# Kernel optimization log

Hardware: AMD Instinct MI355X
Metric: run time of the kernel (lower is better)

Reference implementation:

```python
import jax, jax.numpy as jnp
import numpy as np

GUIDING_LAMBDA = 0.6
N_EXPERT = 4


def setup_inputs() -> dict:
    key = jax.random.key(0)
    ks = jax.random.split(key, 8)
    B, L, H, E = 8, 128, 768, 7
    D = 2 * (H + E + 1)  # 1552 pair-embedding dim
    s = 0.02
    return {
        "utter_repr": jax.random.normal(ks[0], (B, L, H), jnp.float32),
        "speaker_ids": jax.random.randint(ks[1], (B, L), 0, 2),
        "emo_W": jax.random.normal(ks[2], (H, E), jnp.float32) * s,
        "emo_b": jnp.zeros((E,), jnp.float32),
        "gate_W": jax.random.normal(ks[3], (D, N_EXPERT), jnp.float32) * s,
        "gate_b": jnp.zeros((N_EXPERT,), jnp.float32),
        "exp_W1": jax.random.normal(ks[4], (N_EXPERT, D, 256), jnp.float32) * s,
        "exp_b1": jnp.zeros((N_EXPERT, 256), jnp.float32),
        "exp_W2": jax.random.normal(ks[5], (N_EXPERT, 256, 2), jnp.float32) * s,
        "exp_b2": jnp.zeros((N_EXPERT, 2), jnp.float32),
    }


def reference(utter_repr, speaker_ids, emo_W, emo_b, gate_W, gate_b,
              exp_W1, exp_b1, exp_W2, exp_b2):
    B, L, H = utter_repr.shape
    flat = utter_repr.reshape(B * L, H)
    # emotion classification head (dropout = identity in eval)
    emotion_pred = flat @ emo_W + emo_b                      # [B*L, 7]
    spk = speaker_ids.reshape(B * L, 1).astype(flat.dtype)
    concat = jnp.concatenate([flat, emotion_pred, spk], axis=-1)
    concat = concat.reshape(B, L, -1)                        # [B, L, 776]
    # all (t, end_t) pairs with t <= end_t  (vectorized form of the nested loops)
    end_idx, t_idx = np.tril_indices(L)                      # P = L(L+1)/2
    pair = jnp.concatenate([concat[:, t_idx], concat[:, end_idx]], axis=-1)
    pair_flat = pair.reshape(-1, pair.shape[-1])             # [B*P, 1552]
    # gating on detached pair embedding
    gating = jax.nn.softmax(
        jax.lax.stop_gradient(pair_flat) @ gate_W + gate_b, axis=-1)
    # mechanical subtask label (speaker / emotion agreement -> 4-way one-hot)
    s_eq = speaker_ids[:, t_idx] == speaker_ids[:, end_idx]  # [B, P]
    emo = jnp.argmax(emotion_pred.reshape(B, L, -1), axis=-1)
    e_eq = emo[:, t_idx] == emo[:, end_idx]
    lbl = jnp.where(s_eq & e_eq, 0,
                    jnp.where(s_eq, 1, jnp.where(e_eq, 2, 3)))
    label = jax.nn.one_hot(lbl.reshape(-1), N_EXPERT, dtype=pair_flat.dtype)
    gating = GUIDING_LAMBDA * label + (1.0 - GUIDING_LAMBDA) * gating
    # experts: Linear(1552,256) -> Linear(256,2), no activation between
    hidden = jnp.einsum('pd,edh->eph', pair_flat, exp_W1) + exp_b1[:, None, :]
    expert_out = jnp.einsum('eph,ehc->epc', hidden, exp_W2) + exp_b2[:, None, :]
    cause_pred = jnp.einsum('pe,epc->pc', gating, expert_out)  # [B*P, 2]
    return emotion_pred, cause_pred
```

## Files before the change

kernel.cpp:

```cpp
#include <hip/hip_runtime.h>
#include <math.h>

#define B_   8
#define L_   128
#define H_   768
#define E_   7
#define NE_  4
#define HALF_ 776
#define D_   1552
#define PPB_ 8256
#define NROW_ 1024
#define EMO_OUT_ 7168

#define WEFF_OFF 0
#define BEFF_OFF 12416
#define EARG_OFF 12424
#define GLO_OFF  13448
#define GHI_OFF  17544
#define AA_OFF   21640
#define BB_OFF   29832

__global__ __launch_bounds__(256)
void k_weff(const float* __restrict__ w1,
            const float* __restrict__ w2,
            const float* __restrict__ b1,
            const float* __restrict__ b2,
            float* __restrict__ ws) {
    int idx = blockIdx.x * 256 + threadIdx.x;
    if (idx < NE_ * D_) {
        int e = idx / D_, d = idx % D_;
        const float* w1row = w1 + ((size_t)e * D_ + d) * 256;
        const float* w2e   = w2 + e * 512;
        float a0 = 0.f, a1 = 0.f;
        #pragma unroll 8
        for (int h = 0; h < 256; ++h) {
            float x = w1row[h];
            a0 += x * w2e[2 * h];
            a1 += x * w2e[2 * h + 1];
        }
        ws[WEFF_OFF + d * 8 + e * 2 + 0] = a0;
        ws[WEFF_OFF + d * 8 + e * 2 + 1] = a1;
    } else if (idx < NE_ * D_ + 8) {
        int j = idx - NE_ * D_;
        int e = j >> 1, c = j & 1;
        const float* w2e = w2 + e * 512;
        float acc = b2[e * 2 + c];
        for (int h = 0; h < 256; ++h) acc += b1[e * 256 + h] * w2e[2 * h + c];
        ws[BEFF_OFF + j] = acc;
    }
}

__global__ __launch_bounds__(64)
void k_row(const float* __restrict__ utter,
           const int*   __restrict__ spk,
           const float* __restrict__ emoW,
           const float* __restrict__ emoB,
           const float* __restrict__ gateW,
           float* __restrict__ ws,
           float* __restrict__ out) {
    int row  = blockIdx.x;
    int lane = threadIdx.x;
    const float* x = utter + (size_t)row * H_;

    float aemo[E_];
    float ag[24];
    #pragma unroll
    for (int j = 0; j < E_; ++j) aemo[j] = 0.f;
    #pragma unroll
    for (int k = 0; k < 24; ++k) ag[k] = 0.f;

    for (int d = lane; d < H_; d += 64) {
        float v = x[d];
        const float* ew = emoW + d * E_;
        #pragma unroll
        for (int j = 0; j < E_; ++j) aemo[j] += v * ew[j];
        const float* gl = gateW + d * NE_;
        const float* gh = gateW + (HALF_ + d) * NE_;
        #pragma unroll
        for (int k = 0; k < NE_; ++k) { ag[k] += v * gl[k]; ag[4 + k] += v * gh[k]; }
        const float* wl = ws + WEFF_OFF + d * 8;
        const float* wh = ws + WEFF_OFF + (HALF_ + d) * 8;
        #pragma unroll
        for (int k = 0; k < 8; ++k) { ag[8 + k] += v * wl[k]; ag[16 + k] += v * wh[k]; }
    }

    #pragma unroll
    for (int j = 0; j < E_; ++j) {
        float v = aemo[j];
        for (int o = 32; o > 0; o >>= 1) v += __shfl_xor(v, o, 64);
        aemo[j] = v + emoB[j];
    }

    if (lane == 0) {
        int best = 0; float bv = aemo[0];
        #pragma unroll
        for (int j = 1; j < E_; ++j) if (aemo[j] > bv) { bv = aemo[j]; best = j; }
        ((int*)ws)[EARG_OFF + row] = best;
        #pragma unroll
        for (int j = 0; j < E_; ++j) out[row * E_ + j] = aemo[j];
    }

    if (lane < 8) {
        float v = (lane < E_) ? aemo[lane] : (float)spk[row];
        int d = H_ + lane;
        const float* gl = gateW + d * NE_;
        const float* gh = gateW + (HALF_ + d) * NE_;
        #pragma unroll
        for (int k = 0; k < NE_; ++k) { ag[k] += v * gl[k]; ag[4 + k] += v * gh[k]; }
        const float* wl = ws + WEFF_OFF + d * 8;
        const float* wh = ws + WEFF_OFF + (HALF_ + d) * 8;
        #pragma unroll
        for (int k = 0; k < 8; ++k) { ag[8 + k] += v * wl[k]; ag[16 + k] += v * wh[k]; }
    }

    #pragma unroll
    for (int k = 0; k < 24; ++k) {
        float v = ag[k];
        for (int o = 32; o > 0; o >>= 1) v += __shfl_xor(v, o, 64);
        ag[k] = v;
    }

    if (lane == 0) {
        #pragma unroll
        for (int k = 0; k < NE_; ++k) {
            ws[GLO_OFF + row * 4 + k] = ag[k];
            ws[GHI_OFF + row * 4 + k] = ag[4 + k];
        }
        #pragma unroll
        for (int k = 0; k < 8; ++k) {
            ws[AA_OFF + row * 8 + k] = ag[8 + k];
            ws[BB_OFF + row * 8 + k] = ag[16 + k];
        }
    }
}

__global__ __launch_bounds__(128)
void k_pair(const int* __restrict__ spk,
            const float* __restrict__ ws,
            const float* __restrict__ gate_b,
            float* __restrict__ out) {
    int b   = blockIdx.x >> 7;
    int end = blockIdx.x & 127;
    int t   = threadIdx.x;
    if (t > end) return;

    int rt = b * L_ + t;
    int re = b * L_ + end;

    float gb0 = gate_b[0], gb1 = gate_b[1], gb2 = gate_b[2], gb3 = gate_b[3];
    const float* beff = ws + BEFF_OFF;
    float be[8];
    #pragma unroll
    for (int k = 0; k < 8; ++k) be[k] = beff[k];

    const float* glo = ws + GLO_OFF + rt * 4;
    const float* ghi = ws + GHI_OFF + re * 4;
    float lg[NE_];
    lg[0] = glo[0] + ghi[0] + gb0;
    lg[1] = glo[1] + ghi[1] + gb1;
    lg[2] = glo[2] + ghi[2] + gb2;
    lg[3] = glo[3] + ghi[3] + gb3;

    float m = fmaxf(fmaxf(lg[0], lg[1]), fmaxf(lg[2], lg[3]));
    float ex[NE_], s = 0.f;
    #pragma unroll
    for (int k = 0; k < NE_; ++k) { ex[k] = expf(lg[k] - m); s += ex[k]; }
    float inv = 0.4f / s;

    const int* earg = (const int*)ws + EARG_OFF;
    bool seq = (spk[rt] == spk[re]);
    bool eeq = (earg[rt] == earg[re]);
    int lbl = (seq && eeq) ? 0 : (seq ? 1 : (eeq ? 2 : 3));

    const float* A  = ws + AA_OFF + rt * 8;
    const float* Bv = ws + BB_OFF + re * 8;

    float o0 = 0.f, o1 = 0.f;
    #pragma unroll
    for (int e = 0; e < NE_; ++e) {
        float g = ex[e] * inv + ((e == lbl) ? 0.6f : 0.f);
        o0 += g * (A[e * 2 + 0] + Bv[e * 2 + 0] + be[e * 2 + 0]);
        o1 += g * (A[e * 2 + 1] + Bv[e * 2 + 1] + be[e * 2 + 1]);
    }

    int p = ((end * (end + 1)) >> 1) + t;
    float* cp = out + EMO_OUT_ + ((size_t)b * PPB_ + p) * 2;
    cp[0] = o0;
    cp[1] = o1;
}

extern "C" void kernel_launch(void* const* d_in, const int* in_sizes, int n_in,
                              void* d_out, int out_size, void* d_ws, size_t ws_size,
                              hipStream_t stream) {
    const float* utter = (const float*)d_in[0];
    const int*   spk   = (const int*)  d_in[1];
    const float* emoW  = (const float*)d_in[2];
    const float* emoB  = (const float*)d_in[3];
    const float* gateW = (const float*)d_in[4];
    const float* gateB = (const float*)d_in[5];
    const float* w1    = (const float*)d_in[6];
    const float* b1    = (const float*)d_in[7];
    const float* w2    = (const float*)d_in[8];
    const float* b2    = (const float*)d_in[9];

    float* ws  = (float*)d_ws;
    float* out = (float*)d_out;

    k_weff<<<(NE_ * D_ + 8 + 255) / 256, 256, 0, stream>>>(w1, w2, b1, b2, ws);
    k_row<<<NROW_, 64, 0, stream>>>(utter, spk, emoW, emoB, gateW, ws, out);
    k_pair<<<B_ * L_, 128, 0, stream>>>(spk, ws, gateB, out);
}
```

Measured before the change: 102.4 us.

## Split weff reduction across threads and vectorize row and pair loads

k_weff now gives each (expert, d) output four threads that each cover a quarter of the hidden dimension with float4 loads, then combine the partial sums through shared memory. The bias-folding block is split across eight lanes with a shuffle reduction. k_row processes four contiguous features per lane using float4 loads of the inputs and weights, and k_pair reads its workspace data as float4. The aim is to cut the serial per-thread loop in k_weff, which reads the 6 MB W1 with a strided, uncoalesced pattern, and to reduce the number of load instructions. The cost is higher register use in k_row.

```diff
diff --git a/kernel.cpp b/kernel.cpp
--- a/kernel.cpp
+++ b/kernel.cpp
@@ -20,33 +20,58 @@
 #define AA_OFF   21640
 #define BB_OFF   29832
 
+#define WEFF_BLOCKS 97
+
 __global__ __launch_bounds__(256)
 void k_weff(const float* __restrict__ w1,
             const float* __restrict__ w2,
             const float* __restrict__ b1,
             const float* __restrict__ b2,
             float* __restrict__ ws) {
-    int idx = blockIdx.x * 256 + threadIdx.x;
-    if (idx < NE_ * D_) {
+    int blk = blockIdx.x;
+    if (blk < WEFF_BLOCKS) {
+        __shared__ float red[4][64][2];
+        int dl = threadIdx.x & 63;
+        int hc = threadIdx.x >> 6;
+        int idx = blk * 64 + dl;
         int e = idx / D_, d = idx % D_;
-        const float* w1row = w1 + ((size_t)e * D_ + d) * 256;
-        const float* w2e   = w2 + e * 512;
+        const float* w1row = w1 + ((size_t)e * D_ + d) * 256 + hc * 64;
+        const float* w2e   = w2 + e * 512 + hc * 128;
         float a0 = 0.f, a1 = 0.f;
-        #pragma unroll 8
-        for (int h = 0; h < 256; ++h) {
-            float x = w1row[h];
-            a0 += x * w2e[2 * h];
-            a1 += x * w2e[2 * h + 1];
-        }
-        ws[WEFF_OFF + d * 8 + e * 2 + 0] = a0;
-        ws[WEFF_OFF + d * 8 + e * 2 + 1] = a1;
-    } else if (idx < NE_ * D_ + 8) {
-        int j = idx - NE_ * D_;
-        int e = j >> 1, c = j & 1;
-        const float* w2e = w2 + e * 512;
-        float acc = b2[e * 2 + c];
-        for (int h = 0; h < 256; ++h) acc += b1[e * 256 + h] * w2e[2 * h + c];
-        ws[BEFF_OFF + j] = acc;
+        #pragma unroll
+        for (int h = 0; h < 64; h += 4) {
+            float4 wv = *(const float4*)(w1row + h);
+            float4 p0 = *(const float4*)(w2e + 2 * h);
+            float4 p1 = *(const float4*)(w2e + 2 * h + 4);
+            a0 += wv.x * p0.x + wv.y * p0.z + wv.z * p1.x + wv.w * p1.z;
+            a1 += wv.x * p0.y + wv.y * p0.w + wv.z * p1.y + wv.w * p1.w;
+        }
+        red[hc][dl][0] = a0;
+        red[hc][dl][1] = a1;
+        __syncthreads();
+        if (hc == 0) {
+            float s0 = red[0][dl][0] + red[1][dl][0] + red[2][dl][0] + red[3][dl][0];
+            float s1 = red[0][dl][1] + red[1][dl][1] + red[2][dl][1] + red[3][dl][1];
+            ws[WEFF_OFF + d * 8 + e * 2 + 0] = s0;
+            ws[WEFF_OFF + d * 8 + e * 2 + 1] = s1;
+        }
+    } else {
+        int lane = threadIdx.x;
+        if (lane < 64) {
+            int j = lane >> 3;
+            int part = lane & 7;
+            int e = j >> 1, c = j & 1;
+            const float* w2e = w2 + e * 512;
+            const float* b1e = b1 + e * 256;
+            float acc = 0.f;
+            #pragma unroll 8
+            for (int h = part * 32; h < part * 32 + 32; ++h)
+                acc += b1e[h] * w2e[2 * h + c];
+            acc += __shfl_down(acc, 4, 64);
+            acc += __shfl_down(acc, 2, 64);
+            acc += __shfl_down(acc, 1, 64);
+            if (part == 0) ws[BEFF_OFF + j] = acc + b2[j];
+        }
     }
 }
 
@@ -69,19 +94,64 @@
     #pragma unroll
     for (int k = 0; k < 24; ++k) ag[k] = 0.f;
 
-    for (int d = lane; d < H_; d += 64) {
-        float v = x[d];
+    #pragma unroll
+    for (int i = 0; i < 3; ++i) {
+        int d = i * 256 + lane * 4;
+        float4 xv = *(const float4*)(x + d);
+        float xr[4] = {xv.x, xv.y, xv.z, xv.w};
+
+        float ewf[28];
         const float* ew = emoW + d * E_;
         #pragma unroll
-        for (int j = 0; j < E_; ++j) aemo[j] += v * ew[j];
-        const float* gl = gateW + d * NE_;
-        const float* gh = gateW + (HALF_ + d) * NE_;
-        #pragma unroll
-        for (int k = 0; k < NE_; ++k) { ag[k] += v * gl[k]; ag[4 + k] += v * gh[k]; }
-        const float* wl = ws + WEFF_OFF + d * 8;
-        const float* wh = ws + WEFF_OFF + (HALF_ + d) * 8;
-        #pragma unroll
-        for (int k = 0; k < 8; ++k) { ag[8 + k] += v * wl[k]; ag[16 + k] += v * wh[k]; }
+        for (int q = 0; q < 7; ++q) {
+            float4 t = *(const float4*)(ew + q * 4);
+            ewf[q * 4 + 0] = t.x; ewf[q * 4 + 1] = t.y;
+            ewf[q * 4 + 2] = t.z; ewf[q * 4 + 3] = t.w;
+        }
+        #pragma unroll
+        for (int r = 0; r < 4; ++r)
+            #pragma unroll
+            for (int j = 0; j < E_; ++j) aemo[j] += xr[r] * ewf[r * 7 + j];
+
+        float gl[16], gh[16];
+        const float* glp = gateW + d * NE_;
+        const float* ghp = gateW + (HALF_ + d) * NE_;
+        #pragma unroll
+        for (int q = 0; q < 4; ++q) {
+            float4 t0 = *(const float4*)(glp + q * 4);
+            gl[q * 4 + 0] = t0.x; gl[q * 4 + 1] = t0.y;
+            gl[q * 4 + 2] = t0.z; gl[q * 4 + 3] = t0.w;
+            float4 t1 = *(const float4*)(ghp + q * 4);
+            gh[q * 4 + 0] = t1.x; gh[q * 4 + 1] = t1.y;
+            gh[q * 4 + 2] = t1.z; gh[q * 4 + 3] = t1.w;
+        }
+        #pragma unroll
+        for (int r = 0; r < 4; ++r)
+            #pragma unroll
+            for (int k = 0; k < NE_; ++k) {
+                ag[k]     += xr[r] * gl[r * 4 + k];
+                ag[4 + k] += xr[r] * gh[r * 4 + k];
+            }
+
+        float wl[32], wh[32];
+        const float* wlp = ws + WEFF_OFF + d * 8;
+        const float* whp = ws + WEFF_OFF + (HALF_ + d) * 8;
+        #pragma unroll
+        for (int q = 0; q < 8; ++q) {
+            float4 t0 = *(const float4*)(wlp + q * 4);
+            wl[q * 4 + 0] = t0.x; wl[q * 4 + 1] = t0.y;
+            wl[q * 4 + 2] = t0.z; wl[q * 4 + 3] = t0.w;
+            float4 t1 = *(const float4*)(whp + q * 4);
+            wh[q * 4 + 0] = t1.x; wh[q * 4 + 1] = t1.y;
+            wh[q * 4 + 2] = t1.z; wh[q * 4 + 3] = t1.w;
+        }
+        #pragma unroll
+        for (int r = 0; r < 4; ++r)
+            #pragma unroll
+            for (int k = 0; k < 8; ++k) {
+                ag[8 + k]  += xr[r] * wl[r * 8 + k];
+                ag[16 + k] += xr[r] * wh[r * 8 + k];
+            }
     }
 
     #pragma unroll
@@ -103,14 +173,14 @@
     if (lane < 8) {
         float v = (lane < E_) ? aemo[lane] : (float)spk[row];
         int d = H_ + lane;
-        const float* gl = gateW + d * NE_;
-        const float* gh = gateW + (HALF_ + d) * NE_;
-        #pragma unroll
-        for (int k = 0; k < NE_; ++k) { ag[k] += v * gl[k]; ag[4 + k] += v * gh[k]; }
-        const float* wl = ws + WEFF_OFF + d * 8;
-        const float* wh = ws + WEFF_OFF + (HALF_ + d) * 8;
-        #pragma unroll
-        for (int k = 0; k < 8; ++k) { ag[8 + k] += v * wl[k]; ag[16 + k] += v * wh[k]; }
+        const float* glp = gateW + d * NE_;
+        const float* ghp = gateW + (HALF_ + d) * NE_;
+        #pragma unroll
+        for (int k = 0; k < NE_; ++k) { ag[k] += v * glp[k]; ag[4 + k] += v * ghp[k]; }
+        const float* wlp = ws + WEFF_OFF + d * 8;
+        const float* whp = ws + WEFF_OFF + (HALF_ + d) * 8;
+        #pragma unroll
+        for (int k = 0; k < 8; ++k) { ag[8 + k] += v * wlp[k]; ag[16 + k] += v * whp[k]; }
     }
 
     #pragma unroll
@@ -147,19 +217,19 @@
     int rt = b * L_ + t;
     int re = b * L_ + end;
 
-    float gb0 = gate_b[0], gb1 = gate_b[1], gb2 = gate_b[2], gb3 = gate_b[3];
-    const float* beff = ws + BEFF_OFF;
+    float gb[4] = {gate_b[0], gate_b[1], gate_b[2], gate_b[3]};
     float be[8];
-    #pragma unroll
-    for (int k = 0; k < 8; ++k) be[k] = beff[k];
-
-    const float* glo = ws + GLO_OFF + rt * 4;
-    const float* ghi = ws + GHI_OFF + re * 4;
-    float lg[NE_];
-    lg[0] = glo[0] + ghi[0] + gb0;
-    lg[1] = glo[1] + ghi[1] + gb1;
-    lg[2] = glo[2] + ghi[2] + gb2;
-    lg[3] = glo[3] + ghi[3] + gb3;
+    {
+        float4 b0 = *(const float4*)(ws + BEFF_OFF);
+        float4 b1v = *(const float4*)(ws + BEFF_OFF + 4);
+        be[0]=b0.x; be[1]=b0.y; be[2]=b0.z; be[3]=b0.w;
+        be[4]=b1v.x; be[5]=b1v.y; be[6]=b1v.z; be[7]=b1v.w;
+    }
+
+    float4 glo = *(const float4*)(ws + GLO_OFF + rt * 4);
+    float4 ghi = *(const float4*)(ws + GHI_OFF + re * 4);
+    float lg[NE_] = {glo.x + ghi.x + gb[0], glo.y + ghi.y + gb[1],
+                     glo.z + ghi.z + gb[2], glo.w + ghi.w + gb[3]};
 
     float m = fmaxf(fmaxf(lg[0], lg[1]), fmaxf(lg[2], lg[3]));
     float ex[NE_], s = 0.f;
@@ -172,8 +242,17 @@
     bool eeq = (earg[rt] == earg[re]);
     int lbl = (seq && eeq) ? 0 : (seq ? 1 : (eeq ? 2 : 3));
 
-    const float* A  = ws + AA_OFF + rt * 8;
-    const float* Bv = ws + BB_OFF + re * 8;
+    float A[8], Bv[8];
+    {
+        float4 a0 = *(const float4*)(ws + AA_OFF + rt * 8);
+        float4 a1 = *(const float4*)(ws + AA_OFF + rt * 8 + 4);
+        A[0]=a0.x; A[1]=a0.y; A[2]=a0.z; A[3]=a0.w;
+        A[4]=a1.x; A[5]=a1.y; A[6]=a1.z; A[7]=a1.w;
+        float4 v0 = *(const float4*)(ws + BB_OFF + re * 8);
+        float4 v1 = *(const float4*)(ws + BB_OFF + re * 8 + 4);
+        Bv[0]=v0.x; Bv[1]=v0.y; Bv[2]=v0.z; Bv[3]=v0.w;
+        Bv[4]=v1.x; Bv[5]=v1.y; Bv[6]=v1.z; Bv[7]=v1.w;
+    }
 
     float o0 = 0.f, o1 = 0.f;
     #pragma unroll
@@ -206,7 +285,7 @@
     float* ws  = (float*)d_ws;
     float* out = (float*)d_out;
 
-    k_weff<<<(NE_ * D_ + 8 + 255) / 256, 256, 0, stream>>>(w1, w2, b1, b2, ws);
+    k_weff<<<WEFF_BLOCKS + 1, 256, 0, stream>>>(w1, w2, b1, b2, ws);
     k_row<<<NROW_, 64, 0, stream>>>(utter, spk, emoW, emoB, gateW, ws, out);
     k_pair<<<B_ * L_, 128, 0, stream>>>(spk, ws, gateB, out);
 }
```

After: 95.30 us. 1.07x faster.
